# Kernel tuning notes

Hardware: AMD Instinct MI355X
Metric: run time of the kernel (lower is better)

## Reference

```python
import jax, jax.numpy as jnp
import numpy as np

B, S, D, H = 4, 1024, 512, 8
DH = D // H  # dim_head = 64
LN_EPS = 1e-5
COS_EPS = 1e-8


def setup_inputs() -> dict:
    key = jax.random.key(0)
    ks = jax.random.split(key, 8)
    q = jax.random.normal(ks[0], (B, S, D), dtype=jnp.float32)
    k = jax.random.normal(ks[1], (B, S, D), dtype=jnp.float32)
    v = jax.random.normal(ks[2], (B, S, D), dtype=jnp.float32)
    ln_g = jnp.ones((D,), jnp.float32)
    ln_b = jnp.zeros((D,), jnp.float32)
    W_in = jax.random.normal(ks[3], (D, D), dtype=jnp.float32) / np.sqrt(D)
    W_out = jax.random.normal(ks[4], (D, D), dtype=jnp.float32) / np.sqrt(D)
    b_out = jnp.zeros((D,), jnp.float32)
    cov_w = jnp.float32(0.6)
    var_w = jnp.float32(0.2)
    return {"q": q, "k": k, "v": v, "ln_g": ln_g, "ln_b": ln_b,
            "W_in": W_in, "W_out": W_out, "b_out": b_out,
            "cov_w": cov_w, "var_w": var_w}


def reference(q, k, v, ln_g, ln_b, W_in, W_out, b_out, cov_w, var_w):
    def transform(x):
        # input_layernorm followed by bias-free input_linear
        mu = jnp.mean(x, axis=-1, keepdims=True)
        var = jnp.var(x, axis=-1, keepdims=True)
        xn = (x - mu) * jax.lax.rsqrt(var + LN_EPS) * ln_g + ln_b
        y = xn @ W_in
        # 'q n (h d) -> h q n d'
        return y.reshape(B, S, H, DH).transpose(2, 0, 1, 3)

    f_q = transform(q)  # [h, b, n, d]
    f_k = transform(k)  # [h, b, m, d]
    f_v = transform(v)  # [h, b, m, d]

    # cosine_distance(f_q, f_k^T)
    dots = jnp.einsum('hbnd,hbmd->hbnm', f_q, f_k)
    qn = jnp.linalg.norm(f_q, axis=-1)  # [h, b, n]
    kn = jnp.linalg.norm(f_k, axis=-1)  # [h, b, m]
    cosine_sim = dots / (qn[..., :, None] * kn[..., None, :] + COS_EPS)

    # basic_attention_components
    q_c = f_q - jnp.mean(f_q, axis=-1, keepdims=True)
    k_c = f_k - jnp.mean(f_k, axis=-1, keepdims=True)
    cov_component = jnp.einsum('hbnd,hbmd->hbnm', q_c, k_c) / DH
    q_var = jnp.var(f_q, axis=-1, ddof=1)  # torch.var unbiased=True
    k_var = jnp.var(f_k, axis=-1, ddof=1)
    var_component = (q_var[..., :, None] * k_var[..., None, :]) / DH

    # fixed learned-scalar mixing (dynamic_weight=False path)
    attn = (cov_w * cov_component + var_w * var_component
            + (1.0 - cov_w - var_w) * cosine_sim)

    out = jnp.einsum('hbnm,hbmd->hbnd', attn, f_v)
    # 'h q n d -> q n (h d)'
    out = out.transpose(1, 2, 0, 3).reshape(B, S, D)
    return out @ W_out + b_out
```

## Files before the change

### kernel.cpp

```cpp
#include <hip/hip_runtime.h>


#define R_TOT 4096
#define DD 512
#define HB_N 32

typedef __attribute__((ext_vector_type(8))) short short8;
typedef __attribute__((ext_vector_type(4))) float f32x4;

static __device__ inline unsigned short f2bf(float f) {
    union { float f; unsigned u; } x{f};
    unsigned r = x.u + 0x7fff + ((x.u >> 16) & 1);
    return (unsigned short)(r >> 16);
}

__global__ __launch_bounds__(256) void k1_ln_prep(
    const float* __restrict__ q, const float* __restrict__ k, const float* __restrict__ v,
    const float* __restrict__ ln_g, const float* __restrict__ ln_b,
    const float* __restrict__ Win, const float* __restrict__ Wout,
    unsigned short* __restrict__ xn, unsigned short* __restrict__ WinT,
    unsigned short* __restrict__ WoutT)
{
    int blk = blockIdx.x;
    int t = threadIdx.x;
    if (blk < 3 * R_TOT) {
        const float* src = (blk < R_TOT) ? q : (blk < 2 * R_TOT ? k : v);
        const float* x = src + (size_t)(blk & (R_TOT - 1)) * DD;
        float2 val = *(const float2*)(x + t * 2);
        float s = val.x + val.y;
        float s2 = val.x * val.x + val.y * val.y;
        #pragma unroll
        for (int o = 32; o; o >>= 1) { s += __shfl_xor(s, o); s2 += __shfl_xor(s2, o); }
        __shared__ float red[8];
        int wv = t >> 6;
        if ((t & 63) == 0) { red[wv] = s; red[4 + wv] = s2; }
        __syncthreads();
        s = red[0] + red[1] + red[2] + red[3];
        s2 = red[4] + red[5] + red[6] + red[7];
        float mu = s * (1.f / 512.f);
        float var = s2 * (1.f / 512.f) - mu * mu;
        float rstd = rsqrtf(var + 1e-5f);
        float2 gg = *(const float2*)(ln_g + t * 2);
        float2 bb = *(const float2*)(ln_b + t * 2);
        unsigned short* o = xn + (size_t)blk * DD + t * 2;
        o[0] = f2bf((val.x - mu) * rstd * gg.x + bb.x);
        o[1] = f2bf((val.y - mu) * rstd * gg.y + bb.y);
    } else {
        __shared__ float tl[64][65];
        int bb = blk - 3 * R_TOT;
        const float* src = (bb & 64) ? Wout : Win;
        unsigned short* dst = (bb & 64) ? WoutT : WinT;
        int tile = bb & 63;
        int r0 = (tile >> 3) * 64, c0 = (tile & 7) * 64;
        #pragma unroll
        for (int rep = 0; rep < 16; rep++) {
            int rr = rep * 4 + (t >> 6), cc = t & 63;
            tl[rr][cc] = src[(size_t)(r0 + rr) * DD + c0 + cc];
        }
        __syncthreads();
        #pragma unroll
        for (int rep = 0; rep < 16; rep++) {
            int rr = rep * 4 + (t >> 6), cc = t & 63;
            dst[(size_t)(c0 + rr) * DD + r0 + cc] = f2bf(tl[cc][rr]);
        }
    }
}

__global__ __launch_bounds__(256) void gemm512(
    const unsigned short* __restrict__ A, const unsigned short* __restrict__ Bt,
    float* __restrict__ C, const float* __restrict__ bias)
{
    __shared__ __align__(16) unsigned short As[128][40];
    __shared__ __align__(16) unsigned short Bs[128][40];
    int t = threadIdx.x, lane = t & 63, wv = t >> 6;
    int quad = lane >> 4, l15 = lane & 15;
    int m0 = blockIdx.y * 128, n0 = blockIdx.x * 128;
    int wr = (wv >> 1) * 64, wc = (wv & 1) * 64;
    f32x4 acc[4][4] = {};
    for (int kt = 0; kt < 512; kt += 32) {
        __syncthreads();
        #pragma unroll
        for (int ld = 0; ld < 2; ld++) {
            int id = ld * 256 + t;
            int row = id >> 2, co = (id & 3) * 8;
            *(uint4*)&As[row][co] = *(const uint4*)(A + (size_t)(m0 + row) * 512 + kt + co);
            *(uint4*)&Bs[row][co] = *(const uint4*)(Bt + (size_t)(n0 + row) * 512 + kt + co);
        }
        __syncthreads();
        short8 af[4], bf[4];
        #pragma unroll
        for (int i = 0; i < 4; i++) af[i] = *(const short8*)&As[wr + i * 16 + l15][quad * 8];
        #pragma unroll
        for (int j = 0; j < 4; j++) bf[j] = *(const short8*)&Bs[wc + j * 16 + l15][quad * 8];
        #pragma unroll
        for (int i = 0; i < 4; i++)
            #pragma unroll
            for (int j = 0; j < 4; j++)
                acc[i][j] = __builtin_amdgcn_mfma_f32_16x16x32_bf16(af[i], bf[j], acc[i][j], 0, 0, 0);
    }
    #pragma unroll
    for (int i = 0; i < 4; i++)
        #pragma unroll
        for (int j = 0; j < 4; j++)
            #pragma unroll
            for (int r = 0; r < 4; r++) {
                int rr = m0 + wr + i * 16 + quad * 4 + r;
                int cc = n0 + wc + j * 16 + l15;
                float vv = acc[i][j][r];
                if (bias) vv += bias[cc];
                C[(size_t)rr * 512 + cc] = vv;
            }
}

__global__ __launch_bounds__(256) void k3_qstats(
    const float* __restrict__ f, unsigned short* __restrict__ A2)
{
    int r = blockIdx.x;
    int b = r >> 10, s = r & 1023;
    int t = threadIdx.x, wv = t >> 6, lane = t & 63;
    const float* row = f + (size_t)r * DD;
    for (int h = wv; h < 8; h += 4) {
        float val = row[h * 64 + lane];
        float sum = val, sq = val * val;
        #pragma unroll
        for (int o = 32; o; o >>= 1) { sum += __shfl_xor(sum, o); sq += __shfl_xor(sq, o); }
        float mu = sum * (1.f / 64.f);
        float inv = rsqrtf(fmaxf(sq, 1e-20f));
        float var = (sq - 64.f * mu * mu) * (1.f / 63.f);
        int hb = h * 4 + b;
        unsigned short* ob = A2 + ((size_t)hb * 1024 + s) * 160;
        ob[lane] = f2bf(val);
        ob[64 + lane] = f2bf(val * inv);
        if (lane == 0) { ob[128] = f2bf(var); ob[129] = f2bf(mu); }
        if (lane >= 2 && lane < 32) ob[128 + lane] = 0;
    }
}

__global__ __launch_bounds__(256) void k3b_kv(
    const float* __restrict__ f, unsigned short* __restrict__ Lt,
    unsigned short* __restrict__ Vt)
{
    int hb = blockIdx.x, h = hb >> 2, b = hb & 3;
    int s0 = blockIdx.y * 64;
    int t = threadIdx.x, lane = t & 63, wv = t >> 6;
    __shared__ float ks[64][65];
    __shared__ float vs[64][65];
    __shared__ float red[2][4][64];
    __shared__ float stat[3][64];
    const float* fk = f + ((size_t)R_TOT + b * 1024 + s0) * DD + h * 64;
    const float* fv = f + ((size_t)2 * R_TOT + b * 1024 + s0) * DD + h * 64;
    #pragma unroll
    for (int i = 0; i < 4; i++) {
        int id = i * 256 + t, rw = id >> 4, c4 = (id & 15) * 4;
        *(float4*)&ks[rw][c4] = *(const float4*)(fk + (size_t)rw * DD + c4);
        *(float4*)&vs[rw][c4] = *(const float4*)(fv + (size_t)rw * DD + c4);
    }
    __syncthreads();
    float s1 = 0, s2 = 0;
    #pragma unroll
    for (int i = 0; i < 16; i++) {
        float x = ks[lane][wv * 16 + i];
        s1 += x; s2 += x * x;
    }
    red[0][wv][lane] = s1; red[1][wv][lane] = s2;
    __syncthreads();
    if (t < 64) {
        float a = red[0][0][t] + red[0][1][t] + red[0][2][t] + red[0][3][t];
        float q2 = red[1][0][t] + red[1][1][t] + red[1][2][t] + red[1][3][t];
        float mu = a * (1.f / 64.f);
        stat[0][t] = rsqrtf(fmaxf(q2, 1e-20f));
        stat[1][t] = (q2 - 64.f * mu * mu) * (1.f / 63.f);
        stat[2][t] = mu;
    }
    __syncthreads();
    float inv = stat[0][lane], var = stat[1][lane], mu = stat[2][lane];
    unsigned short* lb = Lt + (size_t)hb * 160 * 1024 + s0 + lane;
    #pragma unroll
    for (int i = 0; i < 40; i++) {
        int r = i * 4 + wv;
        float val;
        if (r < 64) val = ks[lane][r];
        else if (r < 128) val = ks[lane][r - 64] * inv;
        else if (r == 128) val = var;
        else if (r == 129) val = mu;
        else val = 0.f;
        lb[(size_t)r * 1024] = f2bf(val);
    }
    unsigned short* vb = Vt + (size_t)hb * 64 * 1024 + s0 + lane;
    #pragma unroll
    for (int i = 0; i < 16; i++) {
        int r = i * 4 + wv;
        vb[(size_t)r * 1024] = f2bf(vs[lane][r]);
    }
}

__global__ __launch_bounds__(256) void k4_ktv(
    const unsigned short* __restrict__ Lt, const unsigned short* __restrict__ Vt,
    float* __restrict__ Cpart)
{
    int hb = blockIdx.x, kt = blockIdx.y;
    int t = threadIdx.x, lane = t & 63, wv = t >> 6;
    int quad = lane >> 4, l15 = lane & 15;
    __shared__ __align__(16) unsigned short As[160][72];
    __shared__ __align__(16) unsigned short Bs[64][72];
    const unsigned short* Ab = Lt + (size_t)hb * 160 * 1024 + kt * 128;
    const unsigned short* Bb = Vt + (size_t)hb * 64 * 1024 + kt * 128;
    f32x4 acc[10] = {};
    for (int kc = 0; kc < 128; kc += 64) {
        __syncthreads();
        #pragma unroll
        for (int i = 0; i < 5; i++) {
            int id = i * 256 + t;
            int row = id >> 3, co = (id & 7) * 8;
            *(uint4*)&As[row][co] = *(const uint4*)(Ab + (size_t)row * 1024 + kc + co);
        }
        #pragma unroll
        for (int i = 0; i < 2; i++) {
            int id = i * 256 + t;
            int row = id >> 3, co = (id & 7) * 8;
            *(uint4*)&Bs[row][co] = *(const uint4*)(Bb + (size_t)row * 1024 + kc + co);
        }
        __syncthreads();
        #pragma unroll
        for (int kk = 0; kk < 2; kk++) {
            short8 bfrag = *(const short8*)&Bs[wv * 16 + l15][kk * 32 + quad * 8];
            #pragma unroll
            for (int mt = 0; mt < 10; mt++) {
                short8 afrag = *(const short8*)&As[mt * 16 + l15][kk * 32 + quad * 8];
                acc[mt] = __builtin_amdgcn_mfma_f32_16x16x32_bf16(afrag, bfrag, acc[mt], 0, 0, 0);
            }
        }
    }
    float* ob = Cpart + ((size_t)hb * 8 + kt) * (160 * 64);
    #pragma unroll
    for (int mt = 0; mt < 10; mt++)
        #pragma unroll
        for (int r = 0; r < 4; r++)
            ob[(mt * 16 + quad * 4 + r) * 64 + wv * 16 + l15] = acc[mt][r];
}

__global__ __launch_bounds__(256) void k5_reduce(
    const float* __restrict__ Cpart, unsigned short* __restrict__ B2t,
    const float* __restrict__ covp, const float* __restrict__ varp)
{
    int hb = blockIdx.x, t = threadIdx.x;
    float cov = covp[0], vw = varp[0];
    float c1 = cov * (1.f / 64.f), cw = 1.f - cov - vw;
    float vw64 = vw * (1.f / 64.f), c2 = -cov;
    const float* base = Cpart + (size_t)hb * 8 * 10240;
    unsigned short* ob = B2t + (size_t)hb * 10240;
    #pragma unroll 4
    for (int rep = 0; rep < 32; rep++) {
        int o = rep * 256 + t;
        int kk = o >> 6, d = o & 63;
        float s = 0;
        #pragma unroll
        for (int c = 0; c < 8; c++) s += base[c * 10240 + kk * 64 + d];
        ob[d * 160 + kk] = f2bf((kk < 64) ? c1 * s : cw * s);
    }
    if (t < 128) {
        int d = t & 63, which = t >> 6;
        int off = 8192 + which * 64 + d;
        float s = 0;
        #pragma unroll
        for (int c = 0; c < 8; c++) s += base[c * 10240 + off];
        ob[d * 160 + 128 + which] = f2bf(which ? c2 * s : vw64 * s);
    }
    for (int o = t; o < 64 * 30; o += 256) {
        int d = o / 30, kk = 130 + o % 30;
        ob[d * 160 + kk] = 0;
    }
}

__global__ __launch_bounds__(256) void k6_apply(
    const unsigned short* __restrict__ A2, const unsigned short* __restrict__ B2t,
    unsigned short* __restrict__ g)
{
    int hb = blockIdx.y, h = hb >> 2, b = hb & 3;
    int m0 = blockIdx.x * 128;
    int t = threadIdx.x, lane = t & 63, wv = t >> 6;
    int quad = lane >> 4, l15 = lane & 15;
    __shared__ __align__(16) unsigned short As[128][40];
    __shared__ __align__(16) unsigned short Bs[64][40];
    const unsigned short* Ab = A2 + (size_t)hb * 1024 * 160;
    const unsigned short* Bb = B2t + (size_t)hb * 10240;
    f32x4 acc[2][4] = {};
    for (int kt = 0; kt < 160; kt += 32) {
        __syncthreads();
        #pragma unroll
        for (int ld = 0; ld < 2; ld++) {
            int id = ld * 256 + t;
            int row = id >> 2, co = (id & 3) * 8;
            *(uint4*)&As[row][co] = *(const uint4*)(Ab + (size_t)(m0 + row) * 160 + kt + co);
        }
        {
            int row = t >> 2, co = (t & 3) * 8;
            *(uint4*)&Bs[row][co] = *(const uint4*)(Bb + (size_t)row * 160 + kt + co);
        }
        __syncthreads();
        short8 af[2], bf[4];
        #pragma unroll
        for (int i = 0; i < 2; i++) af[i] = *(const short8*)&As[wv * 32 + i * 16 + l15][quad * 8];
        #pragma unroll
        for (int j = 0; j < 4; j++) bf[j] = *(const short8*)&Bs[j * 16 + l15][quad * 8];
        #pragma unroll
        for (int i = 0; i < 2; i++)
            #pragma unroll
            for (int j = 0; j < 4; j++)
                acc[i][j] = __builtin_amdgcn_mfma_f32_16x16x32_bf16(af[i], bf[j], acc[i][j], 0, 0, 0);
    }
    #pragma unroll
    for (int i = 0; i < 2; i++)
        #pragma unroll
        for (int j = 0; j < 4; j++)
            #pragma unroll
            for (int r = 0; r < 4; r++) {
                int rr = m0 + wv * 32 + i * 16 + quad * 4 + r;
                int cc = j * 16 + l15;
                g[((size_t)b * 1024 + rr) * 512 + h * 64 + cc] = f2bf(acc[i][j][r]);
            }
}

extern "C" void kernel_launch(void* const* d_in, const int* in_sizes, int n_in,
                              void* d_out, int out_size, void* d_ws, size_t ws_size,
                              hipStream_t stream)
{
    const float* q    = (const float*)d_in[0];
    const float* k    = (const float*)d_in[1];
    const float* v    = (const float*)d_in[2];
    const float* ln_g = (const float*)d_in[3];
    const float* ln_b = (const float*)d_in[4];
    const float* Win  = (const float*)d_in[5];
    const float* Wout = (const float*)d_in[6];
    const float* bout = (const float*)d_in[7];
    const float* covw = (const float*)d_in[8];
    const float* varw = (const float*)d_in[9];

    char* ws = (char*)d_ws;
    size_t off = 0;
    auto alloc = [&](size_t bytes) { size_t r = off; off += (bytes + 255) & ~(size_t)255; return r; };
    size_t xn_off = alloc((size_t)3 * R_TOT * DD * 2);
    unsigned short* xn    = (unsigned short*)(ws + xn_off);
    unsigned short* A2    = (unsigned short*)(ws + xn_off);
    unsigned short* WinT  = (unsigned short*)(ws + alloc((size_t)DD * DD * 2));
    unsigned short* WoutT = (unsigned short*)(ws + alloc((size_t)DD * DD * 2));
    size_t f_off = alloc((size_t)3 * R_TOT * DD * 4);
    float*          f     = (float*)(ws + f_off);
    float*          Cpart = (float*)(ws + f_off);
    unsigned short* g     = (unsigned short*)(ws + f_off + (size_t)HB_N * 8 * 10240 * 4);
    unsigned short* Lt    = (unsigned short*)(ws + alloc((size_t)HB_N * 160 * 1024 * 2));
    unsigned short* Vt    = (unsigned short*)(ws + alloc((size_t)HB_N * 64 * 1024 * 2));
    unsigned short* B2t   = (unsigned short*)(ws + alloc((size_t)HB_N * 10240 * 2));
    (void)ws_size; (void)in_sizes; (void)n_in; (void)out_size;

    k1_ln_prep<<<3 * R_TOT + 128, 256, 0, stream>>>(q, k, v, ln_g, ln_b, Win, Wout, xn, WinT, WoutT);
    gemm512<<<dim3(4, 96), 256, 0, stream>>>(xn, WinT, f, nullptr);
    k3_qstats<<<R_TOT, 256, 0, stream>>>(f, A2);
    k3b_kv<<<dim3(HB_N, 16), 256, 0, stream>>>(f, Lt, Vt);
    k4_ktv<<<dim3(HB_N, 8), 256, 0, stream>>>(Lt, Vt, Cpart);
    k5_reduce<<<HB_N, 256, 0, stream>>>(Cpart, B2t, covw, varw);
    k6_apply<<<dim3(8, HB_N), 256, 0, stream>>>(A2, B2t, g);
    gemm512<<<dim3(4, 32), 256, 0, stream>>>(g, WoutT, (float*)d_out, bout);
}
```

Before: 177.2 us.

## Fuse per-head stats and K/V transposes into the input projection GEMM epilogue

Replaces the fp32 projection output plus the separate q-stats and k/v-prep kernels with a GEMM epilogue. Each wave computes per-row norm, mean and variance from its accumulators via shuffles, stages bf16 tiles in shared memory, and writes A2, Lt and Vt directly. This removes the round trip of the fp32 intermediate f (about 24 MB) and two kernel launches. In exchange the GEMM grows in shared memory and epilogue work, and the workspace layout is reorganized so buffers no longer alias.

```diff
diff --git a/kernel.cpp b/kernel.cpp
--- a/kernel.cpp
+++ b/kernel.cpp
@@ -12,6 +12,12 @@
     union { float f; unsigned u; } x{f};
     unsigned r = x.u + 0x7fff + ((x.u >> 16) & 1);
     return (unsigned short)(r >> 16);
+}
+
+static __device__ inline unsigned scale2(unsigned u, float a, float b) {
+    float lo = __uint_as_float(u << 16);
+    float hi = __uint_as_float(u & 0xffff0000u);
+    return (unsigned)f2bf(lo * a) | ((unsigned)f2bf(hi * b) << 16);
 }
 
 __global__ __launch_bounds__(256) void k1_ln_prep(
@@ -66,6 +72,145 @@
     }
 }
 
+__global__ __launch_bounds__(256) void gemm_qkv(
+    const unsigned short* __restrict__ A, const unsigned short* __restrict__ Bt,
+    unsigned short* __restrict__ A2, unsigned short* __restrict__ Lt,
+    unsigned short* __restrict__ Vt)
+{
+    __shared__ __align__(16) char smbuf[39936];
+    unsigned short (*As)[40] = (unsigned short(*)[40])smbuf;
+    unsigned short (*Bs)[40] = (unsigned short(*)[40])(smbuf + 10240);
+    int t = threadIdx.x, lane = t & 63, wv = t >> 6;
+    int quad = lane >> 4, l15 = lane & 15;
+    int m0 = blockIdx.y * 128, n0 = blockIdx.x * 128;
+    int wr = (wv >> 1) * 64, wc = (wv & 1) * 64;
+    f32x4 acc[4][4] = {};
+    for (int kt = 0; kt < 512; kt += 32) {
+        __syncthreads();
+        #pragma unroll
+        for (int ld = 0; ld < 2; ld++) {
+            int id = ld * 256 + t;
+            int row = id >> 2, co = (id & 3) * 8;
+            *(uint4*)&As[row][co] = *(const uint4*)(A + (size_t)(m0 + row) * 512 + kt + co);
+            *(uint4*)&Bs[row][co] = *(const uint4*)(Bt + (size_t)(n0 + row) * 512 + kt + co);
+        }
+        __syncthreads();
+        short8 af[4], bf[4];
+        #pragma unroll
+        for (int i = 0; i < 4; i++) af[i] = *(const short8*)&As[wr + i * 16 + l15][quad * 8];
+        #pragma unroll
+        for (int j = 0; j < 4; j++) bf[j] = *(const short8*)&Bs[wc + j * 16 + l15][quad * 8];
+        #pragma unroll
+        for (int i = 0; i < 4; i++)
+            #pragma unroll
+            for (int j = 0; j < 4; j++)
+                acc[i][j] = __builtin_amdgcn_mfma_f32_16x16x32_bf16(af[i], bf[j], acc[i][j], 0, 0, 0);
+    }
+    __syncthreads();
+
+    unsigned short* tile = (unsigned short*)(smbuf + wv * 9216);
+    float* st     = (float*)(smbuf + 36864 + wv * 768);
+    float* st_inv = st;
+    float* st_var = st + 64;
+    float* st_mu  = st + 128;
+
+    int typ  = m0 >> 12;
+    int rloc = (m0 & 4095) + wr;
+    int b = rloc >> 10, sb = rloc & 1023;
+    int h = (n0 + wc) >> 6;
+    int hb = h * 4 + b;
+
+    if (typ < 2) {
+        #pragma unroll
+        for (int i = 0; i < 4; i++)
+            #pragma unroll
+            for (int r = 0; r < 4; r++) {
+                float a0 = acc[i][0][r], a1 = acc[i][1][r], a2 = acc[i][2][r], a3 = acc[i][3][r];
+                float s1 = a0 + a1 + a2 + a3;
+                float s2 = a0 * a0 + a1 * a1 + a2 * a2 + a3 * a3;
+                #pragma unroll
+                for (int o = 1; o < 16; o <<= 1) { s1 += __shfl_xor(s1, o); s2 += __shfl_xor(s2, o); }
+                if (l15 == 0) {
+                    int sl = i * 16 + quad * 4 + r;
+                    float mu = s1 * (1.f / 64.f);
+                    st_inv[sl] = rsqrtf(fmaxf(s2, 1e-20f));
+                    st_var[sl] = (s2 - 64.f * mu * mu) * (1.f / 63.f);
+                    st_mu[sl]  = mu;
+                }
+            }
+    }
+    #pragma unroll
+    for (int i = 0; i < 4; i++)
+        #pragma unroll
+        for (int j = 0; j < 4; j++)
+            #pragma unroll
+            for (int r = 0; r < 4; r++) {
+                int sl = i * 16 + quad * 4 + r, d = j * 16 + l15;
+                unsigned short bv = f2bf(acc[i][j][r]);
+                tile[(typ == 0) ? (sl * 72 + d) : (d * 72 + sl)] = bv;
+            }
+
+    if (typ == 0) {
+        unsigned short* ob = A2 + ((size_t)hb * 1024 + sb) * 160;
+        #pragma unroll
+        for (int it = 0; it < 8; it++) {
+            int sl = it * 8 + (lane >> 3), ch = (lane & 7) * 8;
+            uint4 raw = *(uint4*)&tile[sl * 72 + ch];
+            *(uint4*)(ob + (size_t)sl * 160 + ch) = raw;
+            float iv = st_inv[sl];
+            uint4 o2;
+            o2.x = scale2(raw.x, iv, iv); o2.y = scale2(raw.y, iv, iv);
+            o2.z = scale2(raw.z, iv, iv); o2.w = scale2(raw.w, iv, iv);
+            *(uint4*)(ob + (size_t)sl * 160 + 64 + ch) = o2;
+        }
+        {
+            int sl = lane;
+            uint4 z = {0, 0, 0, 0};
+            uint4 t0 = z;
+            t0.x = (unsigned)f2bf(st_var[sl]) | ((unsigned)f2bf(st_mu[sl]) << 16);
+            unsigned short* p = ob + (size_t)sl * 160 + 128;
+            *(uint4*)p = t0;
+            *(uint4*)(p + 8) = z; *(uint4*)(p + 16) = z; *(uint4*)(p + 24) = z;
+        }
+    } else if (typ == 1) {
+        unsigned short* lb = Lt + (size_t)hb * 160 * 1024 + sb;
+        #pragma unroll
+        for (int it = 0; it < 8; it++) {
+            int d = it * 8 + (lane >> 3), ch = (lane & 7) * 8;
+            uint4 raw = *(uint4*)&tile[d * 72 + ch];
+            *(uint4*)(lb + (size_t)d * 1024 + ch) = raw;
+            const float* ivp = st_inv + ch;
+            uint4 o2;
+            o2.x = scale2(raw.x, ivp[0], ivp[1]); o2.y = scale2(raw.y, ivp[2], ivp[3]);
+            o2.z = scale2(raw.z, ivp[4], ivp[5]); o2.w = scale2(raw.w, ivp[6], ivp[7]);
+            *(uint4*)(lb + (size_t)(64 + d) * 1024 + ch) = o2;
+        }
+        if (lane < 16) {
+            int which = lane >> 3, ch = (lane & 7) * 8;
+            const float* sp = (which ? st_mu : st_var) + ch;
+            uint4 o;
+            o.x = (unsigned)f2bf(sp[0]) | ((unsigned)f2bf(sp[1]) << 16);
+            o.y = (unsigned)f2bf(sp[2]) | ((unsigned)f2bf(sp[3]) << 16);
+            o.z = (unsigned)f2bf(sp[4]) | ((unsigned)f2bf(sp[5]) << 16);
+            o.w = (unsigned)f2bf(sp[6]) | ((unsigned)f2bf(sp[7]) << 16);
+            *(uint4*)(lb + (size_t)(128 + which) * 1024 + ch) = o;
+        }
+        uint4 z = {0, 0, 0, 0};
+        for (int zi = lane; zi < 240; zi += 64) {
+            int d = 130 + (zi >> 3), ch = (zi & 7) * 8;
+            *(uint4*)(lb + (size_t)d * 1024 + ch) = z;
+        }
+    } else {
+        unsigned short* vb = Vt + (size_t)hb * 64 * 1024 + sb;
+        #pragma unroll
+        for (int it = 0; it < 8; it++) {
+            int d = it * 8 + (lane >> 3), ch = (lane & 7) * 8;
+            uint4 raw = *(uint4*)&tile[d * 72 + ch];
+            *(uint4*)(vb + (size_t)d * 1024 + ch) = raw;
+        }
+    }
+}
+
 __global__ __launch_bounds__(256) void gemm512(
     const unsigned short* __restrict__ A, const unsigned short* __restrict__ Bt,
     float* __restrict__ C, const float* __restrict__ bias)
@@ -110,88 +255,6 @@
                 if (bias) vv += bias[cc];
                 C[(size_t)rr * 512 + cc] = vv;
             }
-}
-
-__global__ __launch_bounds__(256) void k3_qstats(
-    const float* __restrict__ f, unsigned short* __restrict__ A2)
-{
-    int r = blockIdx.x;
-    int b = r >> 10, s = r & 1023;
-    int t = threadIdx.x, wv = t >> 6, lane = t & 63;
-    const float* row = f + (size_t)r * DD;
-    for (int h = wv; h < 8; h += 4) {
-        float val = row[h * 64 + lane];
-        float sum = val, sq = val * val;
-        #pragma unroll
-        for (int o = 32; o; o >>= 1) { sum += __shfl_xor(sum, o); sq += __shfl_xor(sq, o); }
-        float mu = sum * (1.f / 64.f);
-        float inv = rsqrtf(fmaxf(sq, 1e-20f));
-        float var = (sq - 64.f * mu * mu) * (1.f / 63.f);
-        int hb = h * 4 + b;
-        unsigned short* ob = A2 + ((size_t)hb * 1024 + s) * 160;
-        ob[lane] = f2bf(val);
-        ob[64 + lane] = f2bf(val * inv);
-        if (lane == 0) { ob[128] = f2bf(var); ob[129] = f2bf(mu); }
-        if (lane >= 2 && lane < 32) ob[128 + lane] = 0;
-    }
-}
-
-__global__ __launch_bounds__(256) void k3b_kv(
-    const float* __restrict__ f, unsigned short* __restrict__ Lt,
-    unsigned short* __restrict__ Vt)
-{
-    int hb = blockIdx.x, h = hb >> 2, b = hb & 3;
-    int s0 = blockIdx.y * 64;
-    int t = threadIdx.x, lane = t & 63, wv = t >> 6;
-    __shared__ float ks[64][65];
-    __shared__ float vs[64][65];
-    __shared__ float red[2][4][64];
-    __shared__ float stat[3][64];
-    const float* fk = f + ((size_t)R_TOT + b * 1024 + s0) * DD + h * 64;
-    const float* fv = f + ((size_t)2 * R_TOT + b * 1024 + s0) * DD + h * 64;
-    #pragma unroll
-    for (int i = 0; i < 4; i++) {
-        int id = i * 256 + t, rw = id >> 4, c4 = (id & 15) * 4;
-        *(float4*)&ks[rw][c4] = *(const float4*)(fk + (size_t)rw * DD + c4);
-        *(float4*)&vs[rw][c4] = *(const float4*)(fv + (size_t)rw * DD + c4);
-    }
-    __syncthreads();
-    float s1 = 0, s2 = 0;
-    #pragma unroll
-    for (int i = 0; i < 16; i++) {
-        float x = ks[lane][wv * 16 + i];
-        s1 += x; s2 += x * x;
-    }
-    red[0][wv][lane] = s1; red[1][wv][lane] = s2;
-    __syncthreads();
-    if (t < 64) {
-        float a = red[0][0][t] + red[0][1][t] + red[0][2][t] + red[0][3][t];
-        float q2 = red[1][0][t] + red[1][1][t] + red[1][2][t] + red[1][3][t];
-        float mu = a * (1.f / 64.f);
-        stat[0][t] = rsqrtf(fmaxf(q2, 1e-20f));
-        stat[1][t] = (q2 - 64.f * mu * mu) * (1.f / 63.f);
-        stat[2][t] = mu;
-    }
-    __syncthreads();
-    float inv = stat[0][lane], var = stat[1][lane], mu = stat[2][lane];
-    unsigned short* lb = Lt + (size_t)hb * 160 * 1024 + s0 + lane;
-    #pragma unroll
-    for (int i = 0; i < 40; i++) {
-        int r = i * 4 + wv;
-        float val;
-        if (r < 64) val = ks[lane][r];
-        else if (r < 128) val = ks[lane][r - 64] * inv;
-        else if (r == 128) val = var;
-        else if (r == 129) val = mu;
-        else val = 0.f;
-        lb[(size_t)r * 1024] = f2bf(val);
-    }
-    unsigned short* vb = Vt + (size_t)hb * 64 * 1024 + s0 + lane;
-    #pragma unroll
-    for (int i = 0; i < 16; i++) {
-        int r = i * 4 + wv;
-        vb[(size_t)r * 1024] = f2bf(vs[lane][r]);
-    }
 }
 
 __global__ __launch_bounds__(256) void k4_ktv(
@@ -339,24 +402,19 @@
     char* ws = (char*)d_ws;
     size_t off = 0;
     auto alloc = [&](size_t bytes) { size_t r = off; off += (bytes + 255) & ~(size_t)255; return r; };
-    size_t xn_off = alloc((size_t)3 * R_TOT * DD * 2);
-    unsigned short* xn    = (unsigned short*)(ws + xn_off);
-    unsigned short* A2    = (unsigned short*)(ws + xn_off);
+    unsigned short* xn    = (unsigned short*)(ws + alloc((size_t)3 * R_TOT * DD * 2));
     unsigned short* WinT  = (unsigned short*)(ws + alloc((size_t)DD * DD * 2));
     unsigned short* WoutT = (unsigned short*)(ws + alloc((size_t)DD * DD * 2));
-    size_t f_off = alloc((size_t)3 * R_TOT * DD * 4);
-    float*          f     = (float*)(ws + f_off);
-    float*          Cpart = (float*)(ws + f_off);
-    unsigned short* g     = (unsigned short*)(ws + f_off + (size_t)HB_N * 8 * 10240 * 4);
+    unsigned short* A2    = (unsigned short*)(ws + alloc((size_t)HB_N * 1024 * 160 * 2));
     unsigned short* Lt    = (unsigned short*)(ws + alloc((size_t)HB_N * 160 * 1024 * 2));
     unsigned short* Vt    = (unsigned short*)(ws + alloc((size_t)HB_N * 64 * 1024 * 2));
+    float*          Cpart = (float*)(ws + alloc((size_t)HB_N * 8 * 10240 * 4));
+    unsigned short* g     = (unsigned short*)(ws + alloc((size_t)R_TOT * DD * 2));
     unsigned short* B2t   = (unsigned short*)(ws + alloc((size_t)HB_N * 10240 * 2));
     (void)ws_size; (void)in_sizes; (void)n_in; (void)out_size;
 
     k1_ln_prep<<<3 * R_TOT + 128, 256, 0, stream>>>(q, k, v, ln_g, ln_b, Win, Wout, xn, WinT, WoutT);
-    gemm512<<<dim3(4, 96), 256, 0, stream>>>(xn, WinT, f, nullptr);
-    k3_qstats<<<R_TOT, 256, 0, stream>>>(f, A2);
-    k3b_kv<<<dim3(HB_N, 16), 256, 0, stream>>>(f, Lt, Vt);
+    gemm_qkv<<<dim3(4, 96), 256, 0, stream>>>(xn, WinT, A2, Lt, Vt);
     k4_ktv<<<dim3(HB_N, 8), 256, 0, stream>>>(Lt, Vt, Cpart);
     k5_reduce<<<HB_N, 256, 0, stream>>>(Cpart, B2t, covw, varw);
     k6_apply<<<dim3(8, HB_N), 256, 0, stream>>>(A2, B2t, g);
```

Result: faster. 162.7 us (-8.2%).
